# Optimization experiments

Hardware: AMD Instinct MI355X
Metric: run time of the kernel (lower is better)

## Reference

```python
import jax, jax.numpy as jnp
import numpy as np

KH, KW = 79, 69
STD = 5.0


def setup_inputs() -> dict:
    key = jax.random.key(0)
    x = jax.random.normal(key, (32, 512, 512, 1), dtype=jnp.float32)
    return {"x": x}


def reference(x):
    # Uniform 79x69 box filter (constant, not learned), SAME padding, stride 1.
    filt = jnp.full((KH, KW, 1, 1), 1.0 / (KH * KW), dtype=x.dtype)
    mean = jax.lax.conv_general_dilated(
        x, filt,
        window_strides=(1, 1),
        padding='SAME',
        dimension_numbers=('NHWC', 'HWIO', 'NHWC'),
    )
    return (x - mean) / jnp.asarray(STD, dtype=x.dtype)
```

## Files before the change

### kernel.cpp

```cpp
#include <hip/hip_runtime.h>


#define HH   512
#define WW   512
#define NIMG 32
#define RH   39
#define RW   34
#define TH   32
#define SPAN 110
#define LDSW 584
#define NT   512

__device__ __forceinline__ float hsum4(float4 v) { return (v.x + v.y) + (v.z + v.w); }

template<bool INT>
__device__ __forceinline__ float ldv(const float* col, int g) {
    if (INT) return col[(size_t)g * WW];
    return (g >= 0 && g < HH) ? col[(size_t)g * WW] : 0.0f;
}

template<bool INT>
__device__ __forceinline__ void phase1(float (*cs)[LDSW], const float* img,
                                       int gbase, int c) {
    const float* col = img + c;

    float lo[32];
    #pragma unroll
    for (int t = 0; t < 32; ++t) lo[t] = ldv<INT>(col, gbase + t);

    float m0 = 0, m1 = 0, m2 = 0, m3 = 0;
    #pragma unroll
    for (int t = 32; t < 52; t += 4) {
        m0 += ldv<INT>(col, gbase + t + 0);
        m1 += ldv<INT>(col, gbase + t + 1);
        m2 += ldv<INT>(col, gbase + t + 2);
        m3 += ldv<INT>(col, gbase + t + 3);
    }
    m0 += ldv<INT>(col, gbase + 52);
    m1 += ldv<INT>(col, gbase + 53);
    m2 += ldv<INT>(col, gbase + 54);
    float M = (m0 + m1) + (m2 + m3);

    float hi[32];
    #pragma unroll
    for (int t = 0; t < 32; ++t) hi[t] = ldv<INT>(col, gbase + 78 + t);

    float u0 = 0, u1 = 0, u2 = 0, u3 = 0;
    #pragma unroll
    for (int t = 55; t < 75; t += 4) {
        u0 += ldv<INT>(col, gbase + t + 0);
        u1 += ldv<INT>(col, gbase + t + 1);
        u2 += ldv<INT>(col, gbase + t + 2);
        u3 += ldv<INT>(col, gbase + t + 3);
    }
    u0 += ldv<INT>(col, gbase + 75);
    u1 += ldv<INT>(col, gbase + 76);
    u2 += ldv<INT>(col, gbase + 77);
    float U = (u0 + u1) + (u2 + u3);

    #pragma unroll
    for (int k = 0; k < 32; ++k) { U += hi[k]; hi[k] = U; }

    float L = M;
    #pragma unroll
    for (int k = 31; k >= 0; --k) {
        L += lo[k];
        cs[k][34 + c] = L + hi[k];
    }
}

__global__ __launch_bounds__(NT, 4) void fused_kernel(const float* __restrict__ x,
                                                      float* __restrict__ out) {
    __shared__ float cs[TH][LDSW];

    int d   = blockIdx.x;
    int lin = (d & 7) * 64 + (d >> 3);
    int n   = lin >> 4;
    int h0  = (lin & 15) * TH;
    int tid = threadIdx.x;

    const float* img = x + (size_t)n * HH * WW;
    int gbase = h0 - RH;

    for (int i = tid; i < TH * 72; i += NT) {
        int r = i / 72, cc = i - r * 72;
        cs[r][cc < 34 ? cc : 512 + cc] = 0.0f;
    }

    if (gbase >= 0 && gbase + SPAN <= HH) phase1<true >(cs, img, gbase, tid);
    else                                  phase1<false>(cs, img, gbase, tid);
    __syncthreads();

    const float INV = 1.0f / (79.0f * 69.0f);
    int row = tid >> 4;
    int c0  = (tid & 15) * 32;

    const float4* cp = (const float4*)(&cs[row][0] + c0);
    const float4* xp = (const float4*)(img + (size_t)(h0 + row) * WW + c0);
    float4*       op = (float4*)(out + (size_t)n * HH * WW
                                     + (size_t)(h0 + row) * WW + c0);

    float4 xin[8];
    #pragma unroll
    for (int i = 0; i < 8; ++i) xin[i] = xp[i];

    float4 t4 = make_float4(0, 0, 0, 0), u4 = make_float4(0, 0, 0, 0);
    #pragma unroll
    for (int i = 0; i < 16; i += 2) {
        float4 a = cp[i], b = cp[i + 1];
        t4.x += a.x; t4.y += a.y; t4.z += a.z; t4.w += a.w;
        u4.x += b.x; u4.y += b.y; u4.z += b.z; u4.w += b.w;
    }
    float T = hsum4(t4) + hsum4(u4) + hsum4(cp[16]);

    #pragma unroll
    for (int g = 0; g < 8; ++g) {
        float4 vin  = cp[17 + g];
        float4 vout = cp[g];
        float pin0 = vin.x,  pin1 = pin0 + vin.y,
              pin2 = pin1 + vin.z, pin3 = pin2 + vin.w;
        float po0  = vout.x, po1 = po0 + vout.y,
              po2  = po1 + vout.z, po3 = po2 + vout.w;

        float4 xi = xin[g];
        float4 o;
        o.x = (xi.x - (T + pin0)       * INV) * 0.2f;
        o.y = (xi.y - (T + pin1 - po0) * INV) * 0.2f;
        o.z = (xi.z - (T + pin2 - po1) * INV) * 0.2f;
        o.w = (xi.w - (T + pin3 - po2) * INV) * 0.2f;
        op[g] = o;

        T += pin3 - po3;
    }
}

extern "C" void kernel_launch(void* const* d_in, const int* in_sizes, int n_in,
                              void* d_out, int out_size, void* d_ws, size_t ws_size,
                              hipStream_t stream) {
    const float* x   = (const float*)d_in[0];
    float*       out = (float*)d_out;

    int nblocks = NIMG * (HH / TH);
    fused_kernel<<<nblocks, NT, 0, stream>>>(x, out);
}
```

Before: 95.50 us.

## Store column sums as fp16 in padded LDS and double tile height

The vertical column sums in shared memory are now stored as half precision, at a padded column mapping meant to reduce bank conflicts. The halved storage lets a block hold 64 output rows with 1024 threads, split into two 32-row sub-tiles that each run the same vertical pass. The aim is to cut LDS footprint and traffic per output and to change the block count. The risks are fp16 rounding error in the box-filter mean, and that the doubled block size under the existing launch bounds may force register spills, since each thread keeps 64 floats live.

```diff
diff --git a/kernel.cpp b/kernel.cpp
--- a/kernel.cpp
+++ b/kernel.cpp
@@ -1,4 +1,5 @@
 #include <hip/hip_runtime.h>
+#include <hip/hip_fp16.h>
 
 
 #define HH   512
@@ -6,12 +7,11 @@
 #define NIMG 32
 #define RH   39
 #define RW   34
-#define TH   32
-#define SPAN 110
-#define LDSW 584
-#define NT   512
+#define TH   64
+#define NT   1024
+#define LDSW 658
 
-__device__ __forceinline__ float hsum4(float4 v) { return (v.x + v.y) + (v.z + v.w); }
+__device__ __forceinline__ int cmap(int c) { return c + ((c >> 6) << 3); }
 
 template<bool INT>
 __device__ __forceinline__ float ldv(const float* col, int g) {
@@ -20,7 +20,7 @@
 }
 
 template<bool INT>
-__device__ __forceinline__ void phase1(float (*cs)[LDSW], const float* img,
+__device__ __forceinline__ void phase1(__half* csrow, const float* img,
                                        int gbase, int c) {
     const float* col = img + c;
 
@@ -61,44 +61,58 @@
     #pragma unroll
     for (int k = 0; k < 32; ++k) { U += hi[k]; hi[k] = U; }
 
+    int ci = cmap(34 + c);
     float L = M;
     #pragma unroll
     for (int k = 31; k >= 0; --k) {
         L += lo[k];
-        cs[k][34 + c] = L + hi[k];
+        csrow[(size_t)k * LDSW + ci] = __float2half(L + hi[k]);
     }
 }
 
+__device__ __forceinline__ float4 ld4(const __half* row, int cc) {
+    const __half2* p = (const __half2*)(row + cmap(cc));
+    float2 a = __half22float2(p[0]);
+    float2 b = __half22float2(p[1]);
+    return make_float4(a.x, a.y, b.x, b.y);
+}
+
+__device__ __forceinline__ float hsum4(float4 v) { return (v.x + v.y) + (v.z + v.w); }
+
 __global__ __launch_bounds__(NT, 4) void fused_kernel(const float* __restrict__ x,
                                                       float* __restrict__ out) {
-    __shared__ float cs[TH][LDSW];
+    __shared__ __half cs[TH * LDSW];
 
     int d   = blockIdx.x;
-    int lin = (d & 7) * 64 + (d >> 3);
-    int n   = lin >> 4;
-    int h0  = (lin & 15) * TH;
+    int lin = (d & 7) * 32 + (d >> 3);
+    int n   = lin >> 3;
+    int h0  = (lin & 7) * TH;
     int tid = threadIdx.x;
 
     const float* img = x + (size_t)n * HH * WW;
-    int gbase = h0 - RH;
 
     for (int i = tid; i < TH * 72; i += NT) {
-        int r = i / 72, cc = i - r * 72;
-        cs[r][cc < 34 ? cc : 512 + cc] = 0.0f;
+        int r  = i / 72, cc = i - r * 72;
+        int col = (cc < 34) ? cc : (512 + cc);
+        cs[(size_t)r * LDSW + cmap(col)] = __float2half(0.0f);
     }
 
-    if (gbase >= 0 && gbase + SPAN <= HH) phase1<true >(cs, img, gbase, tid);
-    else                                  phase1<false>(cs, img, gbase, tid);
+    int sub = tid >> 9;
+    int c   = tid & 511;
+    int gb  = h0 - RH + 32 * sub;
+    __half* csrow = cs + (size_t)(32 * sub) * LDSW;
+    if (gb >= 0 && gb + 110 <= HH) phase1<true >(csrow, img, gb, c);
+    else                           phase1<false>(csrow, img, gb, c);
     __syncthreads();
 
     const float INV = 1.0f / (79.0f * 69.0f);
     int row = tid >> 4;
     int c0  = (tid & 15) * 32;
 
-    const float4* cp = (const float4*)(&cs[row][0] + c0);
-    const float4* xp = (const float4*)(img + (size_t)(h0 + row) * WW + c0);
-    float4*       op = (float4*)(out + (size_t)n * HH * WW
-                                     + (size_t)(h0 + row) * WW + c0);
+    const __half*  crow = cs + (size_t)row * LDSW;
+    const float4*  xp = (const float4*)(img + (size_t)(h0 + row) * WW + c0);
+    float4*        op = (float4*)(out + (size_t)n * HH * WW
+                                      + (size_t)(h0 + row) * WW + c0);
 
     float4 xin[8];
     #pragma unroll
@@ -107,16 +121,17 @@
     float4 t4 = make_float4(0, 0, 0, 0), u4 = make_float4(0, 0, 0, 0);
     #pragma unroll
     for (int i = 0; i < 16; i += 2) {
-        float4 a = cp[i], b = cp[i + 1];
+        float4 a = ld4(crow, c0 + 4 * i);
+        float4 b = ld4(crow, c0 + 4 * (i + 1));
         t4.x += a.x; t4.y += a.y; t4.z += a.z; t4.w += a.w;
         u4.x += b.x; u4.y += b.y; u4.z += b.z; u4.w += b.w;
     }
-    float T = hsum4(t4) + hsum4(u4) + hsum4(cp[16]);
+    float T = hsum4(t4) + hsum4(u4) + hsum4(ld4(crow, c0 + 64));
 
     #pragma unroll
     for (int g = 0; g < 8; ++g) {
-        float4 vin  = cp[17 + g];
-        float4 vout = cp[g];
+        float4 vin  = ld4(crow, c0 + 68 + 4 * g);
+        float4 vout = ld4(crow, c0 + 4 * g);
         float pin0 = vin.x,  pin1 = pin0 + vin.y,
               pin2 = pin1 + vin.z, pin3 = pin2 + vin.w;
         float po0  = vout.x, po1 = po0 + vout.y,
```

Result: no change. 94.47 us (-1.1%).
